# Optimization experiments

Measured on AMD Instinct MI355X. Metric: run time of the kernel, lower is better.

## Reference

```python
import jax, jax.numpy as jnp
import numpy as np

IN_C = 64
OUT_C = 64
NUM_RELS = 32
N_NODES = 20000
N_EDGES = 50000


def setup_inputs() -> dict:
    key = jax.random.key(0)
    k1, k2, k3, k4, k5, k6, k7 = jax.random.split(key, 7)
    x = jax.random.normal(k1, (N_NODES, IN_C), dtype=jnp.float32)
    edge_index = jax.random.randint(k2, (2, N_EDGES), 0, N_NODES, dtype=jnp.int64)
    edge_type = jax.random.randint(k3, (N_EDGES,), 0, NUM_RELS, dtype=jnp.int64)
    weight_fwd = jax.random.normal(k4, (NUM_RELS, IN_C * OUT_C), dtype=jnp.float32)
    weight_bwd = jax.random.normal(k5, (NUM_RELS, IN_C * OUT_C), dtype=jnp.float32)
    lin_w = jax.random.normal(k6, (OUT_C, IN_C), dtype=jnp.float32) * (1.0 / np.sqrt(IN_C))
    lin_b = jax.random.normal(k7, (OUT_C,), dtype=jnp.float32) * 0.01
    return {"x": x, "edge_index": edge_index, "edge_type": edge_type,
            "weight_fwd": weight_fwd, "weight_bwd": weight_bwd,
            "lin_w": lin_w, "lin_b": lin_b}


def type_gcn_conv(x, src, dst, edge_type, weight_table):
    # degrees[e] = (# edges sharing src[e]) + 1  (faithful to pairwise-compare count)
    n_nodes = x.shape[0]
    counts = jax.ops.segment_sum(jnp.ones(src.shape[0], jnp.float32), src,
                                 num_segments=n_nodes)
    degrees = counts[src] + 1.0                      # [E]
    w = weight_table[edge_type]                      # [E, in*out] gather
    w = w / (jnp.linalg.norm(w, axis=1, keepdims=True) + 0.01)
    w = w / degrees[:, None]
    w = w.reshape(-1, IN_C, OUT_C)                   # [E, in, out]
    msg = jnp.einsum('ei,eio->eo', x[src], w)        # per-edge small matmul
    return jax.ops.segment_sum(msg, dst, num_segments=n_nodes)  # scatter-add at dst


def reference(x, edge_index, edge_type, weight_fwd, weight_bwd, lin_w, lin_b):
    src, dst = edge_index[0], edge_index[1]
    fwd = type_gcn_conv(x, src, dst, edge_type, weight_fwd)
    # backward conv sees reversed edge_index: its src is original dst
    bwd = type_gcn_conv(x, dst, src, edge_type, weight_bwd)
    return x @ lin_w.T + lin_b + fwd + bwd
```

## Files before the change

### kernel.cpp

```cpp
#include <hip/hip_runtime.h>

#define NREL 32

typedef short short8 __attribute__((ext_vector_type(8)));
typedef float f32x4 __attribute__((ext_vector_type(4)));

__device__ inline unsigned short f2bf(float f) {
    union { float f; unsigned u; } u; u.f = f;
    unsigned r = u.u + 0x7FFF + ((u.u >> 16) & 1);
    return (unsigned short)(r >> 16);
}


__global__ __launch_bounds__(256) void setup_kernel(
        const float* __restrict__ x,
        const int* __restrict__ src, const int* __restrict__ dst,
        const int* __restrict__ et,
        const float* __restrict__ wf, const float* __restrict__ wb,
        const float* __restrict__ lw, const float* __restrict__ lb,
        float* __restrict__ cntf, float* __restrict__ cntb,
        int* __restrict__ fill, unsigned short* __restrict__ wtb,
        unsigned short* __restrict__ xbf, int2* __restrict__ einfo,
        float* __restrict__ out, int E, int N, int nCountB, int CAP) {
    __shared__ float smem[4 * 8 * 64 + 8];
    int tid = threadIdx.x;
    int b = blockIdx.x;

    if (b < nCountB) {
        int* lh = (int*)smem;
        int* lbase = lh + NREL;
        if (tid < 2 * NREL) lh[tid] = 0;
        __syncthreads();
        int e = b * 256 + tid;
        int s = 0, d = 0, r = 0, my = 0;
        bool valid = (e < E);
        if (valid) {
            s = src[e]; d = dst[e]; r = et[e];
            atomicAdd(&cntf[s], 1.0f);
            atomicAdd(&cntb[d], 1.0f);
            my = atomicAdd(&lh[r], 1);
        }
        __syncthreads();
        if (tid < NREL && lh[tid]) lbase[tid] = atomicAdd(&fill[tid], lh[tid]);
        __syncthreads();
        if (valid) einfo[r * CAP + lbase[r] + my] = make_int2(s, d);
        return;
    }
    b -= nCountB;
    if (b < 64) {
        int rel = b & 31, tab = b >> 5;
        const float* s_ = (tab ? wb : wf) + rel * 4096;
        unsigned short* d_ = wtb + (size_t)b * 4096;
        float* part = smem;
        float ssum = 0.f;
        #pragma unroll
        for (int k = 0; k < 16; k += 4) {
            float4 v = *(const float4*)(s_ + tid * 16 + k);
            ssum += v.x * v.x + v.y * v.y + v.z * v.z + v.w * v.w;
        }
        #pragma unroll
        for (int off = 32; off >= 1; off >>= 1) ssum += __shfl_down(ssum, off, 64);
        if ((tid & 63) == 0) part[tid >> 6] = ssum;
        __syncthreads();
        if (tid == 0) part[4] = 1.0f / (sqrtf(part[0] + part[1] + part[2] + part[3]) + 0.01f);
        __syncthreads();
        float sc = part[4];
        int i = tid >> 2, o0 = (tid & 3) * 16;
        #pragma unroll
        for (int q = 0; q < 4; ++q) {
            float4 v = *(const float4*)(s_ + i * 64 + o0 + q * 4);
            d_[(o0 + q * 4 + 0) * 64 + i] = f2bf(v.x * sc);
            d_[(o0 + q * 4 + 1) * 64 + i] = f2bf(v.y * sc);
            d_[(o0 + q * 4 + 2) * 64 + i] = f2bf(v.z * sc);
            d_[(o0 + q * 4 + 3) * 64 + i] = f2bf(v.w * sc);
        }
        return;
    }
    b -= 64;
    {
        int lane = tid & 63, w = tid >> 6;
        int nodeBase = b * 32 + w * 8;
        float4 wrow[16];
        const float4* lwrow = (const float4*)(lw + lane * 64);
        #pragma unroll
        for (int g = 0; g < 16; ++g) wrow[g] = lwrow[g];
        float bias = lb[lane];
        float* xs = smem + w * 8 * 64;
        #pragma unroll
        for (int t = 0; t < 8; ++t) {
            int n = nodeBase + t;
            if (n < N) {
                float v = x[(size_t)n * 64 + lane];
                xs[t * 64 + lane] = v;
                xbf[(size_t)n * 64 + lane] = f2bf(v);
            }
        }
        __syncthreads();
        for (int t = 0; t < 8; ++t) {
            int n = nodeBase + t;
            if (n >= N) break;
            float acc = bias;
            const float4* xr = (const float4*)(xs + t * 64);
            #pragma unroll
            for (int g = 0; g < 16; ++g) {
                float4 xv = xr[g];
                acc = fmaf(xv.x, wrow[g].x, acc);
                acc = fmaf(xv.y, wrow[g].y, acc);
                acc = fmaf(xv.z, wrow[g].z, acc);
                acc = fmaf(xv.w, wrow[g].w, acc);
            }
            out[(size_t)n * 64 + lane] = acc;
        }
    }
}

#define APITCH 72
__global__ __launch_bounds__(256) void conv_mfma(
        const unsigned short* __restrict__ xbf,
        const float* __restrict__ cntf, const float* __restrict__ cntb,
        const int* __restrict__ fill,
        const unsigned short* __restrict__ wtb,
        const int2* __restrict__ einfo,
        float* __restrict__ out, int CAP) {
    int tid = threadIdx.x;
    int lane = tid & 63;

    int fr = (lane < NREL) ? fill[lane] : 0;
    int ch = (fr + 63) >> 6;
    int s_scan = ch;
    #pragma unroll
    for (int off = 1; off < 32; off <<= 1) {
        int t = __shfl_up(s_scan, off, 64);
        if ((lane & 31) >= off) s_scan += t;
    }
    int chExcl = s_scan - ch;

    int c = blockIdx.x;
    unsigned long long mm = __ballot(lane < NREL && c >= chExcl && c < chExcl + ch);
    if (mm == 0) return;
    int rel = __ffsll(mm) - 1;
    int lc = c - __shfl(chExcl, rel, 64);
    int frr = __shfl(fr, rel, 64);
    int pos = rel * CAP + lc * 64;
    int valid = frr - lc * 64;
    if (valid > 64) valid = 64;
    int dir = blockIdx.y;

    __shared__ unsigned short As[64 * APITCH];
    __shared__ unsigned short Bs[64 * APITCH];
    __shared__ int dstS[64];
    __shared__ float invS[64];

    int j = tid >> 2, part = tid & 3;

    {
        const uint4* s4 = (const uint4*)(wtb + (size_t)((dir << 5) + rel) * 4096 + j * 64 + part * 16);
        uint4 v0 = s4[0], v1 = s4[1];
        *(uint4*)(&Bs[j * APITCH + part * 16]) = v0;
        *(uint4*)(&Bs[j * APITCH + part * 16 + 8]) = v1;
    }

    if (j >= valid) {
        uint4 z = {0, 0, 0, 0};
        *(uint4*)(&As[j * APITCH + part * 16]) = z;
        *(uint4*)(&As[j * APITCH + part * 16 + 8]) = z;
        if (part == 0) { dstS[j] = -1; invS[j] = 0.f; }
    } else {
        int2 v = einfo[pos + j];
        int s_ = dir ? v.y : v.x;
        int d_ = dir ? v.x : v.y;
        const uint4* xr = (const uint4*)(xbf + (size_t)s_ * 64);
        uint4 a0 = xr[part * 2], a1 = xr[part * 2 + 1];
        *(uint4*)(&As[j * APITCH + part * 16]) = a0;
        *(uint4*)(&As[j * APITCH + part * 16 + 8]) = a1;
        if (part == 0) {
            float cv = dir ? cntb[s_] : cntf[s_];
            dstS[j] = d_;
            invS[j] = 1.0f / (cv + 1.0f);
        }
    }
    __syncthreads();

    int w = tid >> 6;
    int m = lane & 15, quad = lane >> 4;
    f32x4 acc0 = {0.f, 0.f, 0.f, 0.f}, acc1 = acc0, acc2 = acc0, acc3 = acc0;
    #pragma unroll
    for (int k0 = 0; k0 < 64; k0 += 32) {
        short8 a  = *(const short8*)(&As[(w * 16 + m) * APITCH + k0 + quad * 8]);
        short8 b0 = *(const short8*)(&Bs[(0  + m) * APITCH + k0 + quad * 8]);
        short8 b1 = *(const short8*)(&Bs[(16 + m) * APITCH + k0 + quad * 8]);
        short8 b2 = *(const short8*)(&Bs[(32 + m) * APITCH + k0 + quad * 8]);
        short8 b3 = *(const short8*)(&Bs[(48 + m) * APITCH + k0 + quad * 8]);
        acc0 = __builtin_amdgcn_mfma_f32_16x16x32_bf16(a, b0, acc0, 0, 0, 0);
        acc1 = __builtin_amdgcn_mfma_f32_16x16x32_bf16(a, b1, acc1, 0, 0, 0);
        acc2 = __builtin_amdgcn_mfma_f32_16x16x32_bf16(a, b2, acc2, 0, 0, 0);
        acc3 = __builtin_amdgcn_mfma_f32_16x16x32_bf16(a, b3, acc3, 0, 0, 0);
    }

    int row_base = w * 16 + quad * 4;
    #pragma unroll
    for (int r = 0; r < 4; ++r) {
        int row = row_base + r;
        int d_ = dstS[row];
        if (d_ >= 0) {
            float inv = invS[row];
            float* op = out + (size_t)d_ * 64 + m;
            atomicAdd(op +  0, acc0[r] * inv);
            atomicAdd(op + 16, acc1[r] * inv);
            atomicAdd(op + 32, acc2[r] * inv);
            atomicAdd(op + 48, acc3[r] * inv);
        }
    }
}

extern "C" void kernel_launch(void* const* d_in, const int* in_sizes, int n_in,
                              void* d_out, int out_size, void* d_ws, size_t ws_size,
                              hipStream_t stream) {
    const float* x  = (const float*)d_in[0];
    const int*   ei = (const int*)  d_in[1];
    const int*   et = (const int*)  d_in[2];
    const float* wf = (const float*)d_in[3];
    const float* wb = (const float*)d_in[4];
    const float* lw = (const float*)d_in[5];
    const float* lb = (const float*)d_in[6];
    float* out = (float*)d_out;

    const int E = in_sizes[2];
    const int N = in_sizes[0] / 64;
    const int CAP = ((E + 63) >> 6) << 6;
    const int maxC = ((E + 63) >> 6) + NREL;

    char* p = (char*)d_ws;
    unsigned short* wtb = (unsigned short*)p;  p += (size_t)2 * NREL * 4096 * sizeof(unsigned short);
    unsigned short* xbf = (unsigned short*)p;  p += (size_t)N * 64 * sizeof(unsigned short);
    float* cntf = (float*)p;                   p += (size_t)N * sizeof(float);
    float* cntb = (float*)p;                   p += (size_t)N * sizeof(float);
    int*   fill = (int*)p;                     p += NREL * sizeof(int);
    int2*  einfo = (int2*)p;                   p += (size_t)NREL * CAP * sizeof(int2);

    const int* srcp = ei;
    const int* dstp = ei + E;

    hipMemsetAsync(cntf, 0, ((size_t)2 * N + NREL) * sizeof(float), stream);

    const int nCountB = (E + 255) / 256;
    const int nLinB   = (N + 31) / 32;
    setup_kernel<<<nCountB + 64 + nLinB, 256, 0, stream>>>(
        x, srcp, dstp, et, wf, wb, lw, lb, cntf, cntb, fill, wtb, xbf, einfo,
        out, E, N, nCountB, CAP);
    dim3 cgrid(maxC, 2);
    conv_mfma<<<cgrid, 256, 0, stream>>>(xbf, cntf, cntb, fill, wtb, einfo, out, CAP);
}
```

Measured before the change: 112.2 us.

## Load MFMA operands directly from global memory into registers, dropping LDS staging

The conv kernel no longer stages the gathered x rows and the relation weight tile in shared memory. Each lane now loads its own A and B fragments straight from global memory, and edge metadata (dst, inverse degree) is passed between lanes with shuffles instead of LDS arrays. This removes the LDS writes, the block barrier and the LDS reads. In exchange, each wave separately refetches the 8 KB weight tile through cache, and invalid rows load a duplicate of edge 0 rather than zeros, with their results masked at the atomic stage.

```diff
diff --git a/kernel.cpp b/kernel.cpp
--- a/kernel.cpp
+++ b/kernel.cpp
@@ -114,7 +114,6 @@
     }
 }
 
-#define APITCH 72
 __global__ __launch_bounds__(256) void conv_mfma(
         const unsigned short* __restrict__ xbf,
         const float* __restrict__ cntf, const float* __restrict__ cntb,
@@ -146,69 +145,55 @@
     if (valid > 64) valid = 64;
     int dir = blockIdx.y;
 
-    __shared__ unsigned short As[64 * APITCH];
-    __shared__ unsigned short Bs[64 * APITCH];
-    __shared__ int dstS[64];
-    __shared__ float invS[64];
-
-    int j = tid >> 2, part = tid & 3;
-
+    int w = tid >> 6, m = lane & 15, quad = lane >> 4;
+
+    int row = w * 16 + m;
+    int2 v = einfo[pos + (row < valid ? row : 0)];
+    int s_ = dir ? v.y : v.x;
+    int d_ = dir ? v.x : v.y;
+    float cv = dir ? cntb[s_] : cntf[s_];
+    float inv = 1.0f / (cv + 1.0f);
+
+    const unsigned short* xr = xbf + (size_t)s_ * 64 + quad * 8;
+    short8 a0 = *(const short8*)(xr);
+    short8 a1 = *(const short8*)(xr + 32);
+
+    const unsigned short* bb = wtb + (size_t)((dir << 5) + rel) * 4096
+                                   + m * 64 + quad * 8;
+    f32x4 zero4 = {0.f, 0.f, 0.f, 0.f};
+    f32x4 acc0 = zero4, acc1 = zero4, acc2 = zero4, acc3 = zero4;
     {
-        const uint4* s4 = (const uint4*)(wtb + (size_t)((dir << 5) + rel) * 4096 + j * 64 + part * 16);
-        uint4 v0 = s4[0], v1 = s4[1];
-        *(uint4*)(&Bs[j * APITCH + part * 16]) = v0;
-        *(uint4*)(&Bs[j * APITCH + part * 16 + 8]) = v1;
-    }
-
-    if (j >= valid) {
-        uint4 z = {0, 0, 0, 0};
-        *(uint4*)(&As[j * APITCH + part * 16]) = z;
-        *(uint4*)(&As[j * APITCH + part * 16 + 8]) = z;
-        if (part == 0) { dstS[j] = -1; invS[j] = 0.f; }
-    } else {
-        int2 v = einfo[pos + j];
-        int s_ = dir ? v.y : v.x;
-        int d_ = dir ? v.x : v.y;
-        const uint4* xr = (const uint4*)(xbf + (size_t)s_ * 64);
-        uint4 a0 = xr[part * 2], a1 = xr[part * 2 + 1];
-        *(uint4*)(&As[j * APITCH + part * 16]) = a0;
-        *(uint4*)(&As[j * APITCH + part * 16 + 8]) = a1;
-        if (part == 0) {
-            float cv = dir ? cntb[s_] : cntf[s_];
-            dstS[j] = d_;
-            invS[j] = 1.0f / (cv + 1.0f);
-        }
-    }
-    __syncthreads();
-
-    int w = tid >> 6;
-    int m = lane & 15, quad = lane >> 4;
-    f32x4 acc0 = {0.f, 0.f, 0.f, 0.f}, acc1 = acc0, acc2 = acc0, acc3 = acc0;
-    #pragma unroll
-    for (int k0 = 0; k0 < 64; k0 += 32) {
-        short8 a  = *(const short8*)(&As[(w * 16 + m) * APITCH + k0 + quad * 8]);
-        short8 b0 = *(const short8*)(&Bs[(0  + m) * APITCH + k0 + quad * 8]);
-        short8 b1 = *(const short8*)(&Bs[(16 + m) * APITCH + k0 + quad * 8]);
-        short8 b2 = *(const short8*)(&Bs[(32 + m) * APITCH + k0 + quad * 8]);
-        short8 b3 = *(const short8*)(&Bs[(48 + m) * APITCH + k0 + quad * 8]);
-        acc0 = __builtin_amdgcn_mfma_f32_16x16x32_bf16(a, b0, acc0, 0, 0, 0);
-        acc1 = __builtin_amdgcn_mfma_f32_16x16x32_bf16(a, b1, acc1, 0, 0, 0);
-        acc2 = __builtin_amdgcn_mfma_f32_16x16x32_bf16(a, b2, acc2, 0, 0, 0);
-        acc3 = __builtin_amdgcn_mfma_f32_16x16x32_bf16(a, b3, acc3, 0, 0, 0);
-    }
-
-    int row_base = w * 16 + quad * 4;
+        short8 b0 = *(const short8*)(bb);
+        short8 b1 = *(const short8*)(bb + 1024);
+        short8 b2 = *(const short8*)(bb + 2048);
+        short8 b3 = *(const short8*)(bb + 3072);
+        acc0 = __builtin_amdgcn_mfma_f32_16x16x32_bf16(a0, b0, acc0, 0, 0, 0);
+        acc1 = __builtin_amdgcn_mfma_f32_16x16x32_bf16(a0, b1, acc1, 0, 0, 0);
+        acc2 = __builtin_amdgcn_mfma_f32_16x16x32_bf16(a0, b2, acc2, 0, 0, 0);
+        acc3 = __builtin_amdgcn_mfma_f32_16x16x32_bf16(a0, b3, acc3, 0, 0, 0);
+    }
+    {
+        short8 b0 = *(const short8*)(bb + 32);
+        short8 b1 = *(const short8*)(bb + 1024 + 32);
+        short8 b2 = *(const short8*)(bb + 2048 + 32);
+        short8 b3 = *(const short8*)(bb + 3072 + 32);
+        acc0 = __builtin_amdgcn_mfma_f32_16x16x32_bf16(a1, b0, acc0, 0, 0, 0);
+        acc1 = __builtin_amdgcn_mfma_f32_16x16x32_bf16(a1, b1, acc1, 0, 0, 0);
+        acc2 = __builtin_amdgcn_mfma_f32_16x16x32_bf16(a1, b2, acc2, 0, 0, 0);
+        acc3 = __builtin_amdgcn_mfma_f32_16x16x32_bf16(a1, b3, acc3, 0, 0, 0);
+    }
+
     #pragma unroll
     for (int r = 0; r < 4; ++r) {
-        int row = row_base + r;
-        int d_ = dstS[row];
-        if (d_ >= 0) {
-            float inv = invS[row];
-            float* op = out + (size_t)d_ * 64 + m;
-            atomicAdd(op +  0, acc0[r] * inv);
-            atomicAdd(op + 16, acc1[r] * inv);
-            atomicAdd(op + 32, acc2[r] * inv);
-            atomicAdd(op + 48, acc3[r] * inv);
+        int qq = quad * 4 + r;
+        int dd = __shfl(d_, qq, 64);
+        float iv = __shfl(inv, qq, 64);
+        if (w * 16 + qq < valid) {
+            float* op = out + (size_t)dd * 64 + m;
+            atomicAdd(op +  0, acc0[r] * iv);
+            atomicAdd(op + 16, acc1[r] * iv);
+            atomicAdd(op + 32, acc2[r] * iv);
+            atomicAdd(op + 48, acc3[r] * iv);
         }
     }
 }
```

Measured after the change: 112.9 us. Within noise of the previous version (+0.7%).
